# Kernel optimization log

Measured on AMD Instinct MI355X. Metric: run time of the kernel, lower is better.

## Reference

```python
import jax, jax.numpy as jnp
import numpy as np

HIDDEN = 1024
NUM_HEADS = 16
HEAD_DIM = HIDDEN // NUM_HEADS
BATCH = 2
SEQ = 2048


def setup_inputs() -> dict:
    key = jax.random.key(0)
    k1, k2, k3 = jax.random.split(key, 3)
    hidden_states = jax.random.normal(k1, (BATCH, SEQ, HIDDEN), dtype=jnp.float32)
    attention_mask = jnp.zeros((BATCH, 1, SEQ, SEQ), dtype=jnp.float32)
    # nn.Linear weights: stored as [out_features, in_features]
    w_qkv = jax.random.normal(k2, (3 * HIDDEN, HIDDEN), dtype=jnp.float32) * (HIDDEN ** -0.5)
    w_o = jax.random.normal(k3, (HIDDEN, HIDDEN), dtype=jnp.float32) * (HIDDEN ** -0.5)
    return {"hidden_states": hidden_states, "attention_mask": attention_mask,
            "w_qkv": w_qkv, "w_o": w_o}


def reference(hidden_states, attention_mask, w_qkv, w_o):
    B, S, H = hidden_states.shape
    scale = HEAD_DIM ** -0.5
    qkv = jnp.einsum('bsh,oh->bso', hidden_states, w_qkv)  # [B,S,3H]
    qkv = qkv.reshape(B, S, 3, NUM_HEADS, HEAD_DIM)
    q = qkv[:, :, 0].transpose(0, 2, 1, 3)  # [B,nH,S,hd]
    k = qkv[:, :, 1].transpose(0, 2, 1, 3)
    v = qkv[:, :, 2].transpose(0, 2, 1, 3)
    attn = jnp.einsum('bhqd,bhkd->bhqk', q, k) * scale
    attn = attn + attention_mask
    attn = jax.nn.softmax(attn, axis=-1)
    out = jnp.einsum('bhqk,bhkd->bhqd', attn, v)
    out = out.transpose(0, 2, 1, 3).reshape(B, S, H)
    return jnp.einsum('bsh,oh->bso', out, w_o)
```

## Files before the change

kernel.cpp:

```cpp
#include <hip/hip_runtime.h>

typedef unsigned short u16;
using bf16x8 = __attribute__((ext_vector_type(8))) __bf16;
using f32x4  = __attribute__((ext_vector_type(4))) float;
using u16x8  = __attribute__((ext_vector_type(8))) unsigned short;
using u16x4  = __attribute__((ext_vector_type(4))) unsigned short;

#define SEQ   2048
#define HID   1024
#define NHEAD 16
#define HD    64
#define BATCH 2
#define NTOK  4096

__device__ __forceinline__ u16 f2bf(float f) {
  unsigned u = __builtin_bit_cast(unsigned, f);
  u += 0x7fffu + ((u >> 16) & 1u);
  return (u16)(u >> 16);
}

__device__ __forceinline__ void gld_lds16(const void* g, void* l) {
  __builtin_amdgcn_global_load_lds(
      (__attribute__((address_space(1))) void*)(__UINTPTR_TYPE__)g,
      (__attribute__((address_space(3))) void*)l, 16, 0, 0);
}

__global__ __launch_bounds__(256) void cvt3_kernel(const float* __restrict__ a, u16* __restrict__ oa,
                                                   const float* __restrict__ b, u16* __restrict__ ob,
                                                   const float* __restrict__ c, u16* __restrict__ oc) {
  const float* in; u16* out; int off;
  int bid = blockIdx.x;
  if (bid < 4096)      { in = a; out = oa; off = bid; }
  else if (bid < 7168) { in = b; out = ob; off = bid - 4096; }
  else                 { in = c; out = oc; off = bid - 7168; }
  int i = (off * 256 + threadIdx.x) * 4;
  float4 v = *reinterpret_cast<const float4*>(in + i);
  u16x4 o = { f2bf(v.x), f2bf(v.y), f2bf(v.z), f2bf(v.w) };
  *reinterpret_cast<u16x4*>(out + i) = o;
}

template<bool BF16OUT>
__global__ __launch_bounds__(256) void gemm_bt(const u16* __restrict__ A,
                                               const u16* __restrict__ B,
                                               void* __restrict__ Cv,
                                               int M, int N, int K) {
  __shared__ u16 At[128 * 64];
  __shared__ u16 Bt[128 * 64];
  const int tid  = threadIdx.x;
  const int wave = tid >> 6;
  const int lane = tid & 63;
  const int g    = lane >> 4;
  const int r16  = lane & 15;
  const int wr   = wave >> 1;
  const int wc   = wave & 1;
  const int bm   = blockIdx.y;
  const int bn   = blockIdx.x;

  const u16* Ab = A + (size_t)bm * 128 * K;
  const u16* Bb = B + (size_t)bn * 128 * K;
  const int srow = lane >> 3;
  const int scol = (lane & 7) * 8;

  f32x4 acc[4][4] = {};

  for (int kt = 0; kt < K; kt += 64) {
#pragma unroll
    for (int c = 0; c < 4; ++c) {
      int seg = wave * 4 + c;
      gld_lds16(Ab + (size_t)(seg * 8 + srow) * K + kt + scol, &At[seg * 512]);
      gld_lds16(Bb + (size_t)(seg * 8 + srow) * K + kt + scol, &Bt[seg * 512]);
    }
    __syncthreads();
#pragma unroll
    for (int ko = 0; ko < 64; ko += 32) {
      bf16x8 af[4], bfr[4];
#pragma unroll
      for (int mi = 0; mi < 4; ++mi)
        af[mi] = *reinterpret_cast<const bf16x8*>(&At[(wr * 64 + mi * 16 + r16) * 64 + ko + g * 8]);
#pragma unroll
      for (int ni = 0; ni < 4; ++ni)
        bfr[ni] = *reinterpret_cast<const bf16x8*>(&Bt[(wc * 64 + ni * 16 + r16) * 64 + ko + g * 8]);
#pragma unroll
      for (int mi = 0; mi < 4; ++mi)
#pragma unroll
        for (int ni = 0; ni < 4; ++ni)
          acc[mi][ni] = __builtin_amdgcn_mfma_f32_16x16x32_bf16(af[mi], bfr[ni], acc[mi][ni], 0, 0, 0);
    }
    __syncthreads();
  }

#pragma unroll
  for (int mi = 0; mi < 4; ++mi)
#pragma unroll
    for (int ni = 0; ni < 4; ++ni) {
      int row0 = bm * 128 + wr * 64 + mi * 16 + g * 4;
      int col  = bn * 128 + wc * 64 + ni * 16 + r16;
#pragma unroll
      for (int r = 0; r < 4; ++r) {
        float v = acc[mi][ni][r];
        if (BF16OUT) ((u16*)Cv)[(size_t)(row0 + r) * N + col] = f2bf(v);
        else         ((float*)Cv)[(size_t)(row0 + r) * N + col] = v;
      }
    }
}

__global__ __launch_bounds__(256) void gemm_bt64(const u16* __restrict__ A,
                                                 const u16* __restrict__ B,
                                                 float* __restrict__ C,
                                                 int M, int N, int K) {
  __shared__ u16 At[128 * 64];
  __shared__ u16 Bt[64 * 64];
  const int tid  = threadIdx.x;
  const int wave = tid >> 6;
  const int lane = tid & 63;
  const int g    = lane >> 4;
  const int r16  = lane & 15;
  const int bm   = blockIdx.y;
  const int bn   = blockIdx.x;

  const u16* Ab = A + (size_t)bm * 128 * K;
  const u16* Bb = B + (size_t)bn * 64 * K;
  const int srow = lane >> 3;
  const int scol = (lane & 7) * 8;

  f32x4 acc[2][4] = {};

  for (int kt = 0; kt < K; kt += 64) {
#pragma unroll
    for (int c = 0; c < 4; ++c) {
      int seg = wave * 4 + c;
      gld_lds16(Ab + (size_t)(seg * 8 + srow) * K + kt + scol, &At[seg * 512]);
    }
#pragma unroll
    for (int c = 0; c < 2; ++c) {
      int seg = wave * 2 + c;
      gld_lds16(Bb + (size_t)(seg * 8 + srow) * K + kt + scol, &Bt[seg * 512]);
    }
    __syncthreads();
#pragma unroll
    for (int ko = 0; ko < 64; ko += 32) {
      bf16x8 af[2], bfr[4];
#pragma unroll
      for (int mi = 0; mi < 2; ++mi)
        af[mi] = *reinterpret_cast<const bf16x8*>(&At[(wave * 32 + mi * 16 + r16) * 64 + ko + g * 8]);
#pragma unroll
      for (int ni = 0; ni < 4; ++ni)
        bfr[ni] = *reinterpret_cast<const bf16x8*>(&Bt[(ni * 16 + r16) * 64 + ko + g * 8]);
#pragma unroll
      for (int mi = 0; mi < 2; ++mi)
#pragma unroll
        for (int ni = 0; ni < 4; ++ni)
          acc[mi][ni] = __builtin_amdgcn_mfma_f32_16x16x32_bf16(af[mi], bfr[ni], acc[mi][ni], 0, 0, 0);
    }
    __syncthreads();
  }

#pragma unroll
  for (int mi = 0; mi < 2; ++mi)
#pragma unroll
    for (int ni = 0; ni < 4; ++ni) {
      int row0 = bm * 128 + wave * 32 + mi * 16 + g * 4;
      int col  = bn * 64 + ni * 16 + r16;
#pragma unroll
      for (int r = 0; r < 4; ++r)
        C[(size_t)(row0 + r) * N + col] = acc[mi][ni][r];
    }
}

__global__ __launch_bounds__(256, 4) void attn_kernel(const u16* __restrict__ qkv,
                                                      const float* __restrict__ mask,
                                                      u16* __restrict__ AO) {
  __shared__ u16 Kt[2][64 * 64];
  __shared__ u16 Vt[64 * 64];
  __shared__ u16 Pl[4][16 * 64];

  const int tid  = threadIdx.x;
  const int w    = tid >> 6;
  const int lane = tid & 63;
  const int g    = lane >> 4;
  const int r16  = lane & 15;

  const int n  = blockIdx.x;
  const int x  = n & 7;
  const int s_ = n >> 3;
  const int h  = s_ & 15;
  const int t_ = ((s_ >> 4) << 3) + x;
  const int b  = t_ >> 5;
  const int qt = t_ & 31;

  const size_t tokbase = (size_t)b * SEQ;

  bf16x8 aq[2];
  {
    int qrow = qt * 64 + w * 16 + r16;
#pragma unroll
    for (int ko = 0; ko < 2; ++ko)
      aq[ko] = *reinterpret_cast<const bf16x8*>(
          qkv + ((tokbase + qrow) * 3 + 0) * HID + h * HD + ko * 32 + g * 8);
  }

  f32x4 o[4] = {};
  float mrow[4], lrow[4];
#pragma unroll
  for (int r = 0; r < 4; ++r) { mrow[r] = -3.0e38f; lrow[r] = 0.f; }

  const int srowK = lane >> 3;
  const int vkey  = tid >> 2;
  const int vd3   = tid & 3;

#define STAGE_K(buf, kb)                                                        \
  {                                                                             \
    _Pragma("unroll")                                                           \
    for (int c = 0; c < 2; ++c) {                                               \
      int seg = w * 2 + c;                                                      \
      int sK  = ((seg >> 1) + srowK) & 7;                                       \
      int srcc = (lane & 7) ^ sK;                                               \
      gld_lds16(qkv + ((tokbase + (kb) + seg * 8 + srowK) * 3 + 1) * HID +      \
                    h * HD + srcc * 8,                                          \
                &Kt[buf][seg * 512]);                                           \
    }                                                                           \
  }

  STAGE_K(0, 0);

#pragma unroll 1
  for (int kb = 0; kb < SEQ; kb += 64) {
    const int cur = (kb >> 6) & 1;
    const int nxt = cur ^ 1;
    const bool more = (kb + 64) < SEQ;

    float mpre[4][4];
#pragma unroll
    for (int r = 0; r < 4; ++r) {
      int q = qt * 64 + w * 16 + g * 4 + r;
      const float* mp = mask + ((size_t)b * SEQ + q) * SEQ + kb;
#pragma unroll
      for (int ni = 0; ni < 4; ++ni) mpre[r][ni] = mp[ni * 16 + r16];
    }
    const u16* vp = qkv + ((tokbase + kb + vkey) * 3 + 2) * HID + h * HD + vd3 * 16;
    u16x8 v0 = *reinterpret_cast<const u16x8*>(vp);
    u16x8 v1 = *reinterpret_cast<const u16x8*>(vp + 8);

    __syncthreads();

#pragma unroll
    for (int j = 0; j < 16; ++j) {
      u16 val = (j < 8) ? (u16)v0[j] : (u16)v1[j - 8];
      int row = vd3 * 16 + j;
      int sV  = (vd3 + (j & 7)) & 7;
      Vt[row * 64 + (((vkey >> 3) ^ sV) << 3) + (vkey & 7)] = val;
    }
    __syncthreads();

    f32x4 sf[4] = {};
    __builtin_amdgcn_s_setprio(1);
#pragma unroll
    for (int ko = 0; ko < 2; ++ko) {
      bf16x8 bk[4];
#pragma unroll
      for (int ni = 0; ni < 4; ++ni) {
        int row = ni * 16 + r16;
        int sK  = (ni + (r16 & 7)) & 7;
        bk[ni] = *reinterpret_cast<const bf16x8*>(
            &Kt[cur][row * 64 + (((ko * 4 + g) ^ sK) << 3)]);
      }
#pragma unroll
      for (int ni = 0; ni < 4; ++ni)
        sf[ni] = __builtin_amdgcn_mfma_f32_16x16x32_bf16(aq[ko], bk[ni], sf[ni], 0, 0, 0);
    }
    __builtin_amdgcn_s_setprio(0);

#pragma unroll
    for (int r = 0; r < 4; ++r) {
      float mx = -3.0e38f;
#pragma unroll
      for (int ni = 0; ni < 4; ++ni) {
        float sv = sf[ni][r] * 0.125f + mpre[r][ni];
        sf[ni][r] = sv;
        mx = fmaxf(mx, sv);
      }
      mx = fmaxf(mx, __shfl_xor(mx, 1));
      mx = fmaxf(mx, __shfl_xor(mx, 2));
      mx = fmaxf(mx, __shfl_xor(mx, 4));
      mx = fmaxf(mx, __shfl_xor(mx, 8));
      float mnew  = fmaxf(mrow[r], mx);
      float alpha = __expf(mrow[r] - mnew);
      mrow[r] = mnew;
      float s = 0.f;
#pragma unroll
      for (int ni = 0; ni < 4; ++ni) {
        float p = __expf(sf[ni][r] - mnew);
        sf[ni][r] = p;
        s += p;
      }
      s += __shfl_xor(s, 1); s += __shfl_xor(s, 2);
      s += __shfl_xor(s, 4); s += __shfl_xor(s, 8);
      lrow[r] = lrow[r] * alpha + s;
#pragma unroll
      for (int di = 0; di < 4; ++di) o[di][r] *= alpha;
      int prow = g * 4 + r;
      int sP   = prow & 7;
#pragma unroll
      for (int ni = 0; ni < 4; ++ni) {
        int chunk = ni * 2 + (r16 >> 3);
        Pl[w][prow * 64 + ((chunk ^ sP) << 3) + (r16 & 7)] = f2bf(sf[ni][r]);
      }
    }

    if (more) STAGE_K(nxt, kb + 64);

    __builtin_amdgcn_s_setprio(1);
#pragma unroll
    for (int kk = 0; kk < 2; ++kk) {
      bf16x8 pa, bv[4];
      pa = *reinterpret_cast<const bf16x8*>(
          &Pl[w][r16 * 64 + (((kk * 4 + g) ^ (r16 & 7)) << 3)]);
#pragma unroll
      for (int di = 0; di < 4; ++di) {
        int row = di * 16 + r16;
        int sV  = (di + (r16 & 7)) & 7;
        bv[di] = *reinterpret_cast<const bf16x8*>(
            &Vt[row * 64 + (((kk * 4 + g) ^ sV) << 3)]);
      }
#pragma unroll
      for (int di = 0; di < 4; ++di)
        o[di] = __builtin_amdgcn_mfma_f32_16x16x32_bf16(pa, bv[di], o[di], 0, 0, 0);
    }
    __builtin_amdgcn_s_setprio(0);
  }

#pragma unroll
  for (int di = 0; di < 4; ++di)
#pragma unroll
    for (int r = 0; r < 4; ++r) {
      int srow = qt * 64 + w * 16 + g * 4 + r;
      float val = o[di][r] / lrow[r];
      AO[(tokbase + srow) * HID + h * HD + di * 16 + r16] = f2bf(val);
    }
#undef STAGE_K
}

extern "C" void kernel_launch(void* const* d_in, const int* in_sizes, int n_in,
                              void* d_out, int out_size, void* d_ws, size_t ws_size,
                              hipStream_t stream) {
  (void)in_sizes; (void)n_in; (void)out_size; (void)ws_size;
  const float* hs   = (const float*)d_in[0];
  const float* mask = (const float*)d_in[1];
  const float* wqkv = (const float*)d_in[2];
  const float* wo   = (const float*)d_in[3];
  float* out = (float*)d_out;

  char* ws   = (char*)d_ws;
  u16* Xb    = (u16*)(ws);
  u16* Wqkvb = (u16*)(ws + 8u  * 1024 * 1024);
  u16* Wob   = (u16*)(ws + 14u * 1024 * 1024);
  u16* QKVb  = (u16*)(ws + 16u * 1024 * 1024);
  u16* AOb   = (u16*)(ws + 40u * 1024 * 1024);

  cvt3_kernel<<<8192, 256, 0, stream>>>(hs, Xb, wqkv, Wqkvb, wo, Wob);

  gemm_bt<true><<<dim3(3072 / 128, 4096 / 128), 256, 0, stream>>>(Xb, Wqkvb, QKVb, NTOK, 3072, HID);
  attn_kernel  <<<1024, 256, 0, stream>>>(QKVb, mask, AOb);
  gemm_bt64    <<<dim3(1024 / 64, 4096 / 128), 256, 0, stream>>>(AOb, Wob, out, NTOK, 1024, HID);
}
```

Baseline: 198.3 us.

## Software-prefetch next V tile and mask block in attention loop

Moves the per-iteration global loads of the V tile and attention mask into a register prefetch for the next key block. V is issued after the LDS transpose barrier and the mask after the softmax, so their global latency overlaps with the MFMA work of the current block. It also replaces one __syncthreads with a custom barrier that waits only on LDS counters, and drops the occupancy hint (256,4) from launch bounds. The extra live registers for the prefetched data may raise register pressure, and removing the occupancy hint can lower occupancy.

```diff
diff --git a/kernel.cpp b/kernel.cpp
--- a/kernel.cpp
+++ b/kernel.cpp
@@ -23,6 +23,13 @@
   __builtin_amdgcn_global_load_lds(
       (__attribute__((address_space(1))) void*)(__UINTPTR_TYPE__)g,
       (__attribute__((address_space(3))) void*)l, 16, 0, 0);
+}
+
+__device__ __forceinline__ void lds_barrier() {
+  __builtin_amdgcn_sched_barrier(0);
+  asm volatile("s_waitcnt lgkmcnt(0)" ::: "memory");
+  __builtin_amdgcn_s_barrier();
+  __builtin_amdgcn_sched_barrier(0);
 }
 
 __global__ __launch_bounds__(256) void cvt3_kernel(const float* __restrict__ a, u16* __restrict__ oa,
@@ -167,9 +174,9 @@
     }
 }
 
-__global__ __launch_bounds__(256, 4) void attn_kernel(const u16* __restrict__ qkv,
-                                                      const float* __restrict__ mask,
-                                                      u16* __restrict__ AO) {
+__global__ __launch_bounds__(256) void attn_kernel(const u16* __restrict__ qkv,
+                                                   const float* __restrict__ mask,
+                                                   u16* __restrict__ AO) {
   __shared__ u16 Kt[2][64 * 64];
   __shared__ u16 Vt[64 * 64];
   __shared__ u16 Pl[4][16 * 64];
@@ -222,6 +229,20 @@
   }
 
   STAGE_K(0, 0);
+  float mpre[4][4];
+#pragma unroll
+  for (int r = 0; r < 4; ++r) {
+    int q = qt * 64 + w * 16 + g * 4 + r;
+    const float* mp = mask + ((size_t)b * SEQ + q) * SEQ + 0;
+#pragma unroll
+    for (int ni = 0; ni < 4; ++ni) mpre[r][ni] = mp[ni * 16 + r16];
+  }
+  u16x8 v0, v1;
+  {
+    const u16* vp = qkv + ((tokbase + 0 + vkey) * 3 + 2) * HID + h * HD + vd3 * 16;
+    v0 = *reinterpret_cast<const u16x8*>(vp);
+    v1 = *reinterpret_cast<const u16x8*>(vp + 8);
+  }
 
 #pragma unroll 1
   for (int kb = 0; kb < SEQ; kb += 64) {
@@ -229,18 +250,6 @@
     const int nxt = cur ^ 1;
     const bool more = (kb + 64) < SEQ;
 
-    float mpre[4][4];
-#pragma unroll
-    for (int r = 0; r < 4; ++r) {
-      int q = qt * 64 + w * 16 + g * 4 + r;
-      const float* mp = mask + ((size_t)b * SEQ + q) * SEQ + kb;
-#pragma unroll
-      for (int ni = 0; ni < 4; ++ni) mpre[r][ni] = mp[ni * 16 + r16];
-    }
-    const u16* vp = qkv + ((tokbase + kb + vkey) * 3 + 2) * HID + h * HD + vd3 * 16;
-    u16x8 v0 = *reinterpret_cast<const u16x8*>(vp);
-    u16x8 v1 = *reinterpret_cast<const u16x8*>(vp + 8);
-
     __syncthreads();
 
 #pragma unroll
@@ -250,7 +259,13 @@
       int sV  = (vd3 + (j & 7)) & 7;
       Vt[row * 64 + (((vkey >> 3) ^ sV) << 3) + (vkey & 7)] = val;
     }
-    __syncthreads();
+    lds_barrier();
+
+    if (more) {
+      const u16* vp = qkv + ((tokbase + kb + 64 + vkey) * 3 + 2) * HID + h * HD + vd3 * 16;
+      v0 = *reinterpret_cast<const u16x8*>(vp);
+      v1 = *reinterpret_cast<const u16x8*>(vp + 8);
+    }
 
     f32x4 sf[4] = {};
     __builtin_amdgcn_s_setprio(1);
@@ -304,6 +319,16 @@
       for (int ni = 0; ni < 4; ++ni) {
         int chunk = ni * 2 + (r16 >> 3);
         Pl[w][prow * 64 + ((chunk ^ sP) << 3) + (r16 & 7)] = f2bf(sf[ni][r]);
+      }
+    }
+
+    if (more) {
+#pragma unroll
+      for (int r = 0; r < 4; ++r) {
+        int q = qt * 64 + w * 16 + g * 4 + r;
+        const float* mp = mask + ((size_t)b * SEQ + q) * SEQ + kb + 64;
+#pragma unroll
+        for (int ni = 0; ni < 4; ++ni) mpre[r][ni] = mp[ni * 16 + r16];
       }
     }
 
```

Result: slower. 213.8 us (+7.8%).

## Split attention over two KV halves and merge partial results

Applied to the files above, without the earlier changes.

Runs the attention kernel with the key/value sequence split into two halves, doubling the grid from 1024 to 2048 blocks. Each half writes a normalized partial output in bf16 plus its row max and sum, and a new merge kernel combines them with log-sum-exp weights. The aim is more parallelism and better CU occupancy on a GPU with many CUs. In exchange it adds an extra kernel launch, extra partial-output traffic, and an extra bf16 rounding of the partial outputs. The split path is taken only when the workspace holds at least 57 MiB.

```diff
diff --git a/kernel.cpp b/kernel.cpp
--- a/kernel.cpp
+++ b/kernel.cpp
@@ -17,6 +17,10 @@
   unsigned u = __builtin_bit_cast(unsigned, f);
   u += 0x7fffu + ((u >> 16) & 1u);
   return (u16)(u >> 16);
+}
+__device__ __forceinline__ float bf2f(u16 v) {
+  unsigned u = ((unsigned)v) << 16;
+  return __builtin_bit_cast(float, u);
 }
 
 __device__ __forceinline__ void gld_lds16(const void* g, void* l) {
@@ -167,9 +171,11 @@
     }
 }
 
+template<bool SPLIT>
 __global__ __launch_bounds__(256, 4) void attn_kernel(const u16* __restrict__ qkv,
                                                       const float* __restrict__ mask,
-                                                      u16* __restrict__ AO) {
+                                                      u16* __restrict__ AO,
+                                                      float* __restrict__ ML) {
   __shared__ u16 Kt[2][64 * 64];
   __shared__ u16 Vt[64 * 64];
   __shared__ u16 Pl[4][16 * 64];
@@ -180,7 +186,11 @@
   const int g    = lane >> 4;
   const int r16  = lane & 15;
 
-  const int n  = blockIdx.x;
+  const int n0   = blockIdx.x;
+  const int half = SPLIT ? (n0 >> 10) : 0;
+  const int kv0  = half << 10;
+  const int n    = n0 & 1023;
+
   const int x  = n & 7;
   const int s_ = n >> 3;
   const int h  = s_ & 15;
@@ -189,6 +199,7 @@
   const int qt = t_ & 31;
 
   const size_t tokbase = (size_t)b * SEQ;
+  const int KVEND = SPLIT ? (kv0 + 1024) : SEQ;
 
   bf16x8 aq[2];
   {
@@ -221,13 +232,13 @@
     }                                                                           \
   }
 
-  STAGE_K(0, 0);
+  STAGE_K(0, kv0);
 
 #pragma unroll 1
-  for (int kb = 0; kb < SEQ; kb += 64) {
+  for (int kb = kv0; kb < KVEND; kb += 64) {
     const int cur = (kb >> 6) & 1;
     const int nxt = cur ^ 1;
-    const bool more = (kb + 64) < SEQ;
+    const bool more = (kb + 64) < KVEND;
 
     float mpre[4][4];
 #pragma unroll
@@ -329,21 +340,55 @@
     __builtin_amdgcn_s_setprio(0);
   }
 
+  u16* AOh = AO + (size_t)half * NTOK * HID;
 #pragma unroll
   for (int di = 0; di < 4; ++di)
 #pragma unroll
     for (int r = 0; r < 4; ++r) {
       int srow = qt * 64 + w * 16 + g * 4 + r;
       float val = o[di][r] / lrow[r];
-      AO[(tokbase + srow) * HID + h * HD + di * 16 + r16] = f2bf(val);
-    }
+      AOh[(tokbase + srow) * HID + h * HD + di * 16 + r16] = f2bf(val);
+    }
+  if (SPLIT && r16 == 0) {
+#pragma unroll
+    for (int r = 0; r < 4; ++r) {
+      int srow = qt * 64 + w * 16 + g * 4 + r;
+      size_t mi_ = ((tokbase + srow) * NHEAD + h) * 4 + half * 2;
+      ML[mi_ + 0] = mrow[r];
+      ML[mi_ + 1] = lrow[r];
+    }
+  }
 #undef STAGE_K
+}
+
+__global__ __launch_bounds__(256) void merge_kernel(u16* __restrict__ P0,
+                                                    const u16* __restrict__ P1,
+                                                    const float* __restrict__ ML) {
+  int t  = blockIdx.x * 256 + threadIdx.x;
+  int i  = t >> 3;
+  int d0 = (t & 7) * 8;
+  int tok = i >> 4, h = i & 15;
+  size_t off = (size_t)tok * HID + h * 64 + d0;
+  float m0 = ML[(size_t)i * 4 + 0], l0 = ML[(size_t)i * 4 + 1];
+  float m1 = ML[(size_t)i * 4 + 2], l1 = ML[(size_t)i * 4 + 3];
+  float ms = fmaxf(m0, m1);
+  float w0 = l0 * __expf(m0 - ms);
+  float w1 = l1 * __expf(m1 - ms);
+  float inv = 1.0f / (w0 + w1);
+  w0 *= inv; w1 *= inv;
+  u16x8 a = *reinterpret_cast<const u16x8*>(P0 + off);
+  u16x8 c = *reinterpret_cast<const u16x8*>(P1 + off);
+  u16x8 o;
+#pragma unroll
+  for (int j = 0; j < 8; ++j)
+    o[j] = f2bf(w0 * bf2f((u16)a[j]) + w1 * bf2f((u16)c[j]));
+  *reinterpret_cast<u16x8*>(P0 + off) = o;
 }
 
 extern "C" void kernel_launch(void* const* d_in, const int* in_sizes, int n_in,
                               void* d_out, int out_size, void* d_ws, size_t ws_size,
                               hipStream_t stream) {
-  (void)in_sizes; (void)n_in; (void)out_size; (void)ws_size;
+  (void)in_sizes; (void)n_in; (void)out_size;
   const float* hs   = (const float*)d_in[0];
   const float* mask = (const float*)d_in[1];
   const float* wqkv = (const float*)d_in[2];
@@ -355,11 +400,21 @@
   u16* Wqkvb = (u16*)(ws + 8u  * 1024 * 1024);
   u16* Wob   = (u16*)(ws + 14u * 1024 * 1024);
   u16* QKVb  = (u16*)(ws + 16u * 1024 * 1024);
-  u16* AOb   = (u16*)(ws + 40u * 1024 * 1024);
+  u16* P0    = (u16*)(ws + 40u * 1024 * 1024);
+  u16* P1    = P0 + (size_t)NTOK * HID;
+  float* ML  = (float*)(ws + 56u * 1024 * 1024);
+
+  const bool split = ws_size >= 57u * 1024 * 1024;
 
   cvt3_kernel<<<8192, 256, 0, stream>>>(hs, Xb, wqkv, Wqkvb, wo, Wob);
-
   gemm_bt<true><<<dim3(3072 / 128, 4096 / 128), 256, 0, stream>>>(Xb, Wqkvb, QKVb, NTOK, 3072, HID);
-  attn_kernel  <<<1024, 256, 0, stream>>>(QKVb, mask, AOb);
-  gemm_bt64    <<<dim3(1024 / 64, 4096 / 128), 256, 0, stream>>>(AOb, Wob, out, NTOK, 1024, HID);
-}
+
+  if (split) {
+    attn_kernel<true><<<2048, 256, 0, stream>>>(QKVb, mask, P0, ML);
+    merge_kernel<<<2048, 256, 0, stream>>>(P0, P1, ML);
+  } else {
+    attn_kernel<false><<<1024, 256, 0, stream>>>(QKVb, mask, P0, ML);
+  }
+
+  gemm_bt64<<<dim3(1024 / 64, 4096 / 128), 256, 0, stream>>>(P0, Wob, out, NTOK, 1024, HID);
+}
```

New measurement: 205.4 us. 3.6% more time.
